# Kernel tuning notes

Measured on AMD Instinct MI355X. Metric: run time of the kernel, lower is better.

Reference implementation:

```python
import jax, jax.numpy as jnp
import numpy as np

B, T, D = 4, 1024, 1024
NEXP, TOPK = 8, 2
N = B * T
# eval capacity: floor(TOPK * 2.0 * N / NEXP) = 2048, already even and >= min_capacity
CAP = 2048
LN_EPS = 1e-5


def setup_inputs() -> dict:
    key = jax.random.key(0)
    ks = jax.random.split(key, 4)
    x = jax.random.normal(ks[0], (B, T, D), jnp.float32)
    w_g = jax.random.normal(ks[1], (D, NEXP), jnp.float32) * 0.02
    c_fc = jax.random.normal(ks[2], (NEXP, D, 4 * D), jnp.float32) * 0.02
    c_proj = jax.random.normal(ks[3], (NEXP, 4 * D, D), jnp.float32) * 0.02
    ln_w = jnp.ones((D,), jnp.float32)
    ln_b = jnp.zeros((D,), jnp.float32)
    return {"x": x, "w_g": w_g, "c_fc": c_fc, "c_proj": c_proj, "ln_w": ln_w, "ln_b": ln_b}


def moe_forward(x, w_g, c_fc, c_proj, ln_w, ln_b):
    xf = x.reshape(N, D)
    # --- Router ---
    logits = xf @ w_g                                   # [N, E]
    topk_vals, topk_idx = jax.lax.top_k(logits, TOPK)   # [N, K]
    masked = jnp.full_like(logits, -jnp.inf)
    masked = masked.at[jnp.arange(N)[:, None], topk_idx].set(topk_vals)
    probs = jax.nn.softmax(masked, axis=-1)             # [N, E]

    # capacity-based ranking (slot 0 for all tokens first, then slot 1, ...)
    onehot = jax.nn.one_hot(topk_idx, NEXP, dtype=jnp.int32)     # [N, K, E]
    exp_mask = jnp.transpose(onehot, (1, 0, 2))                  # [K, N, E]
    rank = jnp.cumsum(exp_mask.reshape(TOPK * N, NEXP), axis=0) - 1
    rank = rank.reshape(TOPK, N, NEXP)
    exp_mask = exp_mask * (rank < CAP).astype(jnp.int32)         # drop overflow
    rank_tok = jnp.sum(exp_mask * rank, axis=-1)                 # [K, N]
    exp_w = exp_mask.astype(probs.dtype) * probs[None]           # [K, N, E]
    rank_oh = jax.nn.one_hot(rank_tok, CAP, dtype=probs.dtype)   # [K, N, C]
    cb_weight = jnp.einsum('kne,knc->nec', exp_w, rank_oh)       # [N, E, C]
    sec_mask = (cb_weight != 0).astype(x.dtype)                  # dispatch mask

    # --- dispatch -> experts -> combine ---
    xb = jnp.einsum('nec,nd->ecd', sec_mask, xf)                 # [E, C, D]
    h = jax.nn.gelu(jnp.einsum('ecd,edf->ecf', xb, c_fc), approximate=False)
    eo = jnp.einsum('ecf,efd->ecd', h, c_proj)                   # [E, C, D]
    out = jnp.einsum('nec,ecd->nd', cb_weight, eo)               # [N, D]

    # --- LayerNorm ---
    mu = out.mean(-1, keepdims=True)
    var = out.var(-1, keepdims=True)
    out = (out - mu) / jnp.sqrt(var + LN_EPS) * ln_w + ln_b
    return out.reshape(B, T, D)


def reference(x, w_g, c_fc, c_proj, ln_w, ln_b):
    return moe_forward(x, w_g, c_fc, c_proj, ln_w, ln_b)
```

## Files before the change

kernel.cpp:

```cpp
#include <hip/hip_runtime.h>
#include <math.h>

#define NEXP 8
#define CAP 2048
#define NTOK 4096
#define DDIM 1024
#define FDIM 4096

typedef __bf16 bf16x8 __attribute__((ext_vector_type(8)));
typedef float f32x4 __attribute__((ext_vector_type(4)));
typedef unsigned short u16x8 __attribute__((ext_vector_type(8)));

__device__ __forceinline__ unsigned short f2bf(float f) {
    unsigned int u = __float_as_uint(f);
    u += 0x7FFFu + ((u >> 16) & 1u);
    return (unsigned short)(u >> 16);
}
__device__ __forceinline__ float bf2f(unsigned short h) {
    return __uint_as_float(((unsigned int)h) << 16);
}

__device__ __forceinline__ void gld_lds16(const void* g, void* l) {
    __builtin_amdgcn_global_load_lds((const __attribute__((address_space(1))) void*)g,
                                     (__attribute__((address_space(3))) void*)l, 16, 0, 0);
}

__global__ __launch_bounds__(256) void transpose_cvt64(const float* __restrict__ in,
                                                       unsigned short* __restrict__ out,
                                                       int R, int C) {
    __shared__ float tile[64][65];
    int e = blockIdx.z;
    const float* ip = in + (size_t)e * R * C;
    unsigned short* op = out + (size_t)e * R * C;
    int c0 = blockIdx.x * 64, r0 = blockIdx.y * 64;
    int t = threadIdx.x;
#pragma unroll
    for (int i = 0; i < 4; i++) {
        int rr = i * 16 + (t >> 4);
        int cc = (t & 15) * 4;
        float4 v = *(const float4*)&ip[(size_t)(r0 + rr) * C + c0 + cc];
        tile[rr][cc] = v.x; tile[rr][cc + 1] = v.y; tile[rr][cc + 2] = v.z; tile[rr][cc + 3] = v.w;
    }
    __syncthreads();
    int c = t >> 2, rb = (t & 3) * 16;
    u16x8 o0, o1;
#pragma unroll
    for (int j = 0; j < 8; j++) o0[j] = f2bf(tile[rb + j][c]);
#pragma unroll
    for (int j = 0; j < 8; j++) o1[j] = f2bf(tile[rb + 8 + j][c]);
    unsigned short* dst = op + (size_t)(c0 + c) * R + r0 + rb;
    *(u16x8*)dst = o0;
    *(u16x8*)(dst + 8) = o1;
}

__global__ __launch_bounds__(256) void router_kernel(const float* __restrict__ x,
                                                     const float* __restrict__ wg,
                                                     int2* __restrict__ e01,
                                                     float2* __restrict__ p01) {
    int wid = threadIdx.x >> 6, lane = threadIdx.x & 63;
    int n = blockIdx.x * 4 + wid;
    float acc[8];
#pragma unroll
    for (int i = 0; i < 8; i++) acc[i] = 0.f;
    const float4* xr = (const float4*)(x + (size_t)n * DDIM);
#pragma unroll
    for (int j = 0; j < 4; j++) {
        float4 xv = xr[j * 64 + lane];
        int base = (j * 64 + lane) * 4;
        float xs[4] = {xv.x, xv.y, xv.z, xv.w};
#pragma unroll
        for (int t = 0; t < 4; t++) {
            const float4* wr = (const float4*)(wg + (size_t)(base + t) * 8);
            float4 w0 = wr[0], w1 = wr[1];
            acc[0] += xs[t] * w0.x; acc[1] += xs[t] * w0.y;
            acc[2] += xs[t] * w0.z; acc[3] += xs[t] * w0.w;
            acc[4] += xs[t] * w1.x; acc[5] += xs[t] * w1.y;
            acc[6] += xs[t] * w1.z; acc[7] += xs[t] * w1.w;
        }
    }
#pragma unroll
    for (int off = 32; off > 0; off >>= 1) {
#pragma unroll
        for (int i = 0; i < 8; i++) acc[i] += __shfl_xor(acc[i], off);
    }
    if (lane == 0) {
        int i0 = 0; float v0 = acc[0];
#pragma unroll
        for (int q = 1; q < 8; q++) { if (acc[q] > v0) { v0 = acc[q]; i0 = q; } }
        int i1 = -1; float v1 = -3.0e38f;
#pragma unroll
        for (int q = 0; q < 8; q++) { if (q != i0 && acc[q] > v1) { v1 = acc[q]; i1 = q; } }
        float ea = expf(v0 - v0), eb = expf(v1 - v0);
        float inv = 1.f / (ea + eb);
        e01[n] = make_int2(i0, i1);
        p01[n] = make_float2(ea * inv, eb * inv);
    }
}

__global__ void assign_kernel(const int2* __restrict__ e01, int* __restrict__ counts,
                              int* __restrict__ assign_row, int* __restrict__ tok_slot) {
    int lane = threadIdx.x;
    int base[8];
#pragma unroll
    for (int i = 0; i < 8; i++) base[i] = 0;
    unsigned long long below = ((unsigned long long)1 << lane) - 1ull;
    int2 cur = e01[lane];
    for (int pass = 0; pass < 2; ++pass) {
        for (int t = 0; t < NTOK; t += 64) {
            int n = t + lane;
            int2 nxt;
            if (t + 64 < NTOK) nxt = e01[t + 64 + lane];
            else nxt = (pass == 0) ? e01[lane] : make_int2(0, 0);
            int ex = (pass == 0) ? cur.x : cur.y;
            int slot = -1;
#pragma unroll
            for (int q = 0; q < 8; q++) {
                unsigned long long m = __ballot(ex == q);
                if (ex == q) slot = base[q] + __popcll(m & below);
                base[q] += __popcll(m);
            }
            if (slot < CAP) {
                assign_row[ex * CAP + slot] = n;
                tok_slot[2 * n + pass] = slot;
            } else {
                tok_slot[2 * n + pass] = -1;
            }
            cur = nxt;
        }
    }
    if (lane < 8) counts[lane] = base[lane] > CAP ? CAP : base[lane];
}

__global__ __launch_bounds__(256) void gather_rows(const float* __restrict__ x,
                                                   const int* __restrict__ assign_row,
                                                   const int* __restrict__ counts,
                                                   unsigned short* __restrict__ xg) {
    int e = blockIdx.y;
    int wid = threadIdx.x >> 6, lane = threadIdx.x & 63;
    int slot = blockIdx.x * 4 + wid;
    if (slot >= counts[e]) return;
    int n = assign_row[e * CAP + slot];
    const float4* src = (const float4*)(x + (size_t)n * DDIM);
    unsigned short* dst = xg + ((size_t)e * CAP + slot) * DDIM;
#pragma unroll
    for (int j = 0; j < 4; j++) {
        float4 v = src[j * 64 + lane];
        ushort4 o;
        o.x = f2bf(v.x); o.y = f2bf(v.y); o.z = f2bf(v.z); o.w = f2bf(v.w);
        *(ushort4*)(dst + (size_t)(j * 64 + lane) * 4) = o;
    }
}

template <bool GELU, int KC>
__global__ __launch_bounds__(256, 4) void gemm_db(const unsigned short* __restrict__ A,
                                                  const unsigned short* __restrict__ Bt,
                                                  unsigned short* __restrict__ Cout,
                                                  const int* __restrict__ counts,
                                                  int Ncols, int Ktot) {
    constexpr int ABYTES = 8192;
    constexpr int BUFB = 16384;
    __shared__ __align__(16) char smem[2 * BUFB];

    int gx = gridDim.x, gy = gridDim.y;
    int nwg = gx * gy * gridDim.z;
    int flat = blockIdx.x + gx * (blockIdx.y + gy * blockIdx.z);
    int cpx = nwg >> 3;
    int swz = (flat & 7) * cpx + (flat >> 3);
    int gxy = gx * gy;
    int zz = swz / gxy;
    int r2 = swz - zz * gxy;
    int by = r2 / gx;
    int bx = r2 - by * gx;
    int e = zz / KC, kc = zz % KC;

    int cnt = counts[e];
    int row0 = by * 128;
    if (row0 >= cnt) return;
    int col0 = bx * 128;
    const int Ksub = Ktot / KC;
    const int NT = Ksub >> 5;

    int tid = threadIdx.x;
    int w = tid >> 6, lane = tid & 63;
    int wm = w >> 1, wn = w & 1;

    const unsigned short* Ab = A + ((size_t)e * CAP + row0) * Ktot + (size_t)kc * Ksub;
    const unsigned short* Bb = Bt + ((size_t)e * Ncols + col0) * Ktot + (size_t)kc * Ksub;

    int kel = (((tid & 3) ^ ((tid >> 3) & 3)) * 8);
    int rA = tid >> 2;
    int ldst = tid * 16;

    int a_off[4], b_off[4];
    int c = lane >> 4;
#pragma unroll
    for (int m = 0; m < 4; m++) {
        int row = wm * 64 + m * 16 + (lane & 15);
        a_off[m] = row * 64 + ((c ^ ((row >> 1) & 3)) * 16);
    }
#pragma unroll
    for (int n = 0; n < 4; n++) {
        int row = wn * 64 + n * 16 + (lane & 15);
        b_off[n] = row * 64 + ((c ^ ((row >> 1) & 3)) * 16);
    }

    auto stage = [&](int tt) {
        int bb = (tt & 1) * BUFB;
        size_t kt = (size_t)tt * 32 + kel;
#pragma unroll
        for (int i = 0; i < 2; i++)
            gld_lds16(Ab + (size_t)(i * 64 + rA) * Ktot + kt, smem + bb + i * 4096 + ldst);
#pragma unroll
        for (int i = 0; i < 2; i++)
            gld_lds16(Bb + (size_t)(i * 64 + rA) * Ktot + kt, smem + bb + ABYTES + i * 4096 + ldst);
    };

    f32x4 acc[4][4] = {};

    stage(0);
    __builtin_amdgcn_sched_barrier(0);
    __syncthreads();

    for (int t = 0; t < NT; ++t) {
        const int bb = (t & 1) * BUFB;
        if (t + 1 < NT) stage(t + 1);
        __builtin_amdgcn_sched_barrier(0);
        bf16x8 af[4], bfr[4];
#pragma unroll
        for (int m = 0; m < 4; m++) af[m] = *(const bf16x8*)(smem + bb + a_off[m]);
#pragma unroll
        for (int n = 0; n < 4; n++) bfr[n] = *(const bf16x8*)(smem + bb + ABYTES + b_off[n]);
        __builtin_amdgcn_s_setprio(1);
#pragma unroll
        for (int m = 0; m < 4; m++)
#pragma unroll
            for (int n = 0; n < 4; n++)
                acc[m][n] = __builtin_amdgcn_mfma_f32_16x16x32_bf16(af[m], bfr[n], acc[m][n], 0, 0, 0);
        __builtin_amdgcn_s_setprio(0);
        __syncthreads();
    }

    unsigned short* Cb = Cout + (((size_t)(kc * NEXP + e) * CAP + row0)) * Ncols + col0;
#pragma unroll
    for (int m = 0; m < 4; m++)
#pragma unroll
        for (int n = 0; n < 4; n++)
#pragma unroll
            for (int j = 0; j < 4; j++) {
                int lr = wm * 64 + m * 16 + ((lane >> 4) << 2) + j;
                int lc = wn * 64 + n * 16 + (lane & 15);
                float v = acc[m][n][j];
                if constexpr (GELU) {
                    float g = 0.5f * v * (1.0f + erff(v * 0.70710678118654752f));
                    Cb[(size_t)lr * Ncols + lc] = f2bf(g);
                } else {
                    Cb[(size_t)lr * Ncols + lc] = f2bf(v);
                }
            }
}

__global__ __launch_bounds__(256) void combine_ln_kernel(const unsigned short* __restrict__ pb,
                                                         const int2* __restrict__ e01,
                                                         const float2* __restrict__ p01,
                                                         const int* __restrict__ tok_slot,
                                                         const float* __restrict__ lnw,
                                                         const float* __restrict__ lnb,
                                                         float* __restrict__ out) {
    const size_t PLANE = (size_t)NEXP * CAP * DDIM;
    int n = blockIdx.x, t = threadIdx.x;
    int2 e = e01[n];
    float2 p = p01[n];
    int s0 = tok_slot[2 * n], s1 = tok_slot[2 * n + 1];
    float o0 = 0.f, o1 = 0.f, o2 = 0.f, o3 = 0.f;
    if (s0 >= 0) {
        size_t base = ((size_t)e.x * CAP + s0) * DDIM;
        ushort4 u0 = ((const ushort4*)(pb + base))[t];
        ushort4 u1 = ((const ushort4*)(pb + PLANE + base))[t];
        o0 += p.x * (bf2f(u0.x) + bf2f(u1.x));
        o1 += p.x * (bf2f(u0.y) + bf2f(u1.y));
        o2 += p.x * (bf2f(u0.z) + bf2f(u1.z));
        o3 += p.x * (bf2f(u0.w) + bf2f(u1.w));
    }
    if (s1 >= 0) {
        size_t base = ((size_t)e.y * CAP + s1) * DDIM;
        ushort4 u0 = ((const ushort4*)(pb + base))[t];
        ushort4 u1 = ((const ushort4*)(pb + PLANE + base))[t];
        o0 += p.y * (bf2f(u0.x) + bf2f(u1.x));
        o1 += p.y * (bf2f(u0.y) + bf2f(u1.y));
        o2 += p.y * (bf2f(u0.z) + bf2f(u1.z));
        o3 += p.y * (bf2f(u0.w) + bf2f(u1.w));
    }
    float s = o0 + o1 + o2 + o3;
    float sq = o0 * o0 + o1 * o1 + o2 * o2 + o3 * o3;
#pragma unroll
    for (int off = 32; off > 0; off >>= 1) {
        s += __shfl_xor(s, off);
        sq += __shfl_xor(sq, off);
    }
    __shared__ float red[8];
    int wid = t >> 6, lane = t & 63;
    if (lane == 0) { red[wid] = s; red[4 + wid] = sq; }
    __syncthreads();
    s = red[0] + red[1] + red[2] + red[3];
    sq = red[4] + red[5] + red[6] + red[7];
    float mu = s * (1.f / DDIM);
    float var = sq * (1.f / DDIM) - mu * mu;
    float inv = rsqrtf(var + 1e-5f);
    const float4 w = ((const float4*)lnw)[t];
    const float4 b = ((const float4*)lnb)[t];
    float4 r;
    r.x = (o0 - mu) * inv * w.x + b.x;
    r.y = (o1 - mu) * inv * w.y + b.y;
    r.z = (o2 - mu) * inv * w.z + b.z;
    r.w = (o3 - mu) * inv * w.w + b.w;
    ((float4*)(out + (size_t)n * DDIM))[t] = r;
}

extern "C" void kernel_launch(void* const* d_in, const int* in_sizes, int n_in,
                              void* d_out, int out_size, void* d_ws, size_t ws_size,
                              hipStream_t stream) {
    const float* x   = (const float*)d_in[0];
    const float* wg  = (const float*)d_in[1];
    const float* cfc = (const float*)d_in[2];
    const float* cpr = (const float*)d_in[3];
    const float* lnw = (const float*)d_in[4];
    const float* lnb = (const float*)d_in[5];
    float* out = (float*)d_out;

    char* ws = (char*)d_ws;
    size_t off = 0;
    auto take = [&](size_t b) {
        char* p = ws + off;
        off += (b + 255) & ~(size_t)255;
        return p;
    };
    unsigned short* cfct = (unsigned short*)take((size_t)NEXP * FDIM * DDIM * 2);
    unsigned short* pb = cfct;
    unsigned short* cprt = (unsigned short*)take((size_t)NEXP * DDIM * FDIM * 2);
    unsigned short* xg   = (unsigned short*)take((size_t)NEXP * CAP * DDIM * 2);
    unsigned short* h    = (unsigned short*)take((size_t)NEXP * CAP * FDIM * 2);
    int2*   e01      = (int2*)take(NTOK * sizeof(int2));
    float2* p01      = (float2*)take(NTOK * sizeof(float2));
    int*    tok_slot = (int*)take((size_t)NTOK * 2 * 4);
    int*    assign_row = (int*)take((size_t)NEXP * CAP * 4);
    int*    counts   = (int*)take(256);

    transpose_cvt64<<<dim3(FDIM / 64, DDIM / 64, NEXP), 256, 0, stream>>>(cfc, cfct, DDIM, FDIM);
    transpose_cvt64<<<dim3(DDIM / 64, FDIM / 64, NEXP), 256, 0, stream>>>(cpr, cprt, FDIM, DDIM);
    router_kernel<<<NTOK / 4, 256, 0, stream>>>(x, wg, e01, p01);
    assign_kernel<<<1, 64, 0, stream>>>(e01, counts, assign_row, tok_slot);
    gather_rows<<<dim3(CAP / 4, NEXP), 256, 0, stream>>>(x, assign_row, counts, xg);
    gemm_db<true, 1><<<dim3(FDIM / 128, CAP / 128, NEXP), 256, 0, stream>>>(xg, cfct, h, counts, FDIM, DDIM);
    gemm_db<false, 2><<<dim3(DDIM / 128, CAP / 128, NEXP * 2), 256, 0, stream>>>(h, cprt, pb, counts, DDIM, FDIM);
    combine_ln_kernel<<<NTOK, 256, 0, stream>>>(pb, e01, p01, tok_slot, lnw, lnb, out);
}
```

Baseline: 359.3 us.

## Use 256x256 tiles with 512 threads and triple-buffered LDS pipeline in expert GEMMs

The expert GEMM kernel now uses 256x256 output tiles with 8 waves per block, each wave holding an 8x4 grid of MFMA accumulators. LDS goes from two to three buffers, loads are issued two k-steps ahead, and explicit vmcnt waits with raw s_barrier replace __syncthreads. The intent is more data reuse per LDS load and better hiding of global-load latency. In exchange the block needs 96KB of LDS and uses more registers, so occupancy drops. The FDIM=4096 GEMM launches fewer blocks, which can hurt load balance on a GPU with many CUs.

```diff
diff --git a/kernel.cpp b/kernel.cpp
--- a/kernel.cpp
+++ b/kernel.cpp
@@ -152,14 +152,14 @@
 }
 
 template <bool GELU, int KC>
-__global__ __launch_bounds__(256, 4) void gemm_db(const unsigned short* __restrict__ A,
+__global__ __launch_bounds__(512, 2) void gemm_pc(const unsigned short* __restrict__ A,
                                                   const unsigned short* __restrict__ Bt,
                                                   unsigned short* __restrict__ Cout,
                                                   const int* __restrict__ counts,
                                                   int Ncols, int Ktot) {
-    constexpr int ABYTES = 8192;
-    constexpr int BUFB = 16384;
-    __shared__ __align__(16) char smem[2 * BUFB];
+    constexpr int ABYTES = 16384;
+    constexpr int BUFB = 32768;
+    __shared__ __align__(16) char smem[3 * BUFB];
 
     int gx = gridDim.x, gy = gridDim.y;
     int nwg = gx * gy * gridDim.z;
@@ -174,82 +174,82 @@
     int e = zz / KC, kc = zz % KC;
 
     int cnt = counts[e];
-    int row0 = by * 128;
+    int row0 = by * 256;
     if (row0 >= cnt) return;
-    int col0 = bx * 128;
+    int col0 = bx * 256;
     const int Ksub = Ktot / KC;
-    const int NT = Ksub >> 5;
-
-    int tid = threadIdx.x;
-    int w = tid >> 6, lane = tid & 63;
-    int wm = w >> 1, wn = w & 1;
+    const int NT = Ksub / 32;
+
+    int tid = threadIdx.x, w = tid >> 6, lane = tid & 63;
+    int wm = w >> 2, wn = w & 3;
 
     const unsigned short* Ab = A + ((size_t)e * CAP + row0) * Ktot + (size_t)kc * Ksub;
     const unsigned short* Bb = Bt + ((size_t)e * Ncols + col0) * Ktot + (size_t)kc * Ksub;
 
     int kel = (((tid & 3) ^ ((tid >> 3) & 3)) * 8);
-    int rA = tid >> 2;
-    int ldst = tid * 16;
-
-    int a_off[4], b_off[4];
-    int c = lane >> 4;
-#pragma unroll
-    for (int m = 0; m < 4; m++) {
-        int row = wm * 64 + m * 16 + (lane & 15);
-        a_off[m] = row * 64 + ((c ^ ((row >> 1) & 3)) * 16);
-    }
-#pragma unroll
-    for (int n = 0; n < 4; n++) {
-        int row = wn * 64 + n * 16 + (lane & 15);
-        b_off[n] = row * 64 + ((c ^ ((row >> 1) & 3)) * 16);
+    int aoff[8], boff[4];
+    int c0 = lane >> 4;
+#pragma unroll
+    for (int mq = 0; mq < 8; mq++) {
+        int row = wm * 128 + mq * 16 + (lane & 15);
+        aoff[mq] = row * 64 + ((c0 ^ ((row >> 1) & 3)) << 4);
+    }
+#pragma unroll
+    for (int nq = 0; nq < 4; nq++) {
+        int row = wn * 64 + nq * 16 + (lane & 15);
+        boff[nq] = row * 64 + ((c0 ^ ((row >> 1) & 3)) << 4);
     }
 
     auto stage = [&](int tt) {
-        int bb = (tt & 1) * BUFB;
+        int bb = (tt % 3) * BUFB;
         size_t kt = (size_t)tt * 32 + kel;
 #pragma unroll
         for (int i = 0; i < 2; i++)
-            gld_lds16(Ab + (size_t)(i * 64 + rA) * Ktot + kt, smem + bb + i * 4096 + ldst);
+            gld_lds16(Ab + (size_t)(i * 128 + (tid >> 2)) * Ktot + kt, smem + bb + i * 8192 + tid * 16);
 #pragma unroll
         for (int i = 0; i < 2; i++)
-            gld_lds16(Bb + (size_t)(i * 64 + rA) * Ktot + kt, smem + bb + ABYTES + i * 4096 + ldst);
+            gld_lds16(Bb + (size_t)(i * 128 + (tid >> 2)) * Ktot + kt, smem + bb + ABYTES + i * 8192 + tid * 16);
     };
 
-    f32x4 acc[4][4] = {};
-
-    stage(0);
+    f32x4 acc[8][4] = {};
+
+    stage(0); stage(1);
+    asm volatile("s_waitcnt vmcnt(4) lgkmcnt(0)" ::: "memory");
     __builtin_amdgcn_sched_barrier(0);
-    __syncthreads();
+    __builtin_amdgcn_s_barrier();
 
     for (int t = 0; t < NT; ++t) {
-        const int bb = (t & 1) * BUFB;
-        if (t + 1 < NT) stage(t + 1);
+        const int bb = (t % 3) * BUFB;
+        if (t + 2 < NT) stage(t + 2);
         __builtin_amdgcn_sched_barrier(0);
-        bf16x8 af[4], bfr[4];
-#pragma unroll
-        for (int m = 0; m < 4; m++) af[m] = *(const bf16x8*)(smem + bb + a_off[m]);
-#pragma unroll
-        for (int n = 0; n < 4; n++) bfr[n] = *(const bf16x8*)(smem + bb + ABYTES + b_off[n]);
+        bf16x8 a[8], b[4];
+#pragma unroll
+        for (int mq = 0; mq < 8; mq++) a[mq] = *(const bf16x8*)(smem + bb + aoff[mq]);
+#pragma unroll
+        for (int nq = 0; nq < 4; nq++) b[nq] = *(const bf16x8*)(smem + bb + ABYTES + boff[nq]);
         __builtin_amdgcn_s_setprio(1);
 #pragma unroll
-        for (int m = 0; m < 4; m++)
-#pragma unroll
-            for (int n = 0; n < 4; n++)
-                acc[m][n] = __builtin_amdgcn_mfma_f32_16x16x32_bf16(af[m], bfr[n], acc[m][n], 0, 0, 0);
+        for (int mq = 0; mq < 8; mq++)
+#pragma unroll
+            for (int nq = 0; nq < 4; nq++)
+                acc[mq][nq] = __builtin_amdgcn_mfma_f32_16x16x32_bf16(a[mq], b[nq], acc[mq][nq], 0, 0, 0);
         __builtin_amdgcn_s_setprio(0);
-        __syncthreads();
+        if (t + 2 < NT) asm volatile("s_waitcnt vmcnt(4) lgkmcnt(0)" ::: "memory");
+        else            asm volatile("s_waitcnt vmcnt(0) lgkmcnt(0)" ::: "memory");
+        __builtin_amdgcn_sched_barrier(0);
+        __builtin_amdgcn_s_barrier();
     }
 
     unsigned short* Cb = Cout + (((size_t)(kc * NEXP + e) * CAP + row0)) * Ncols + col0;
 #pragma unroll
-    for (int m = 0; m < 4; m++)
-#pragma unroll
-        for (int n = 0; n < 4; n++)
+    for (int mq = 0; mq < 8; mq++)
+#pragma unroll
+        for (int nq = 0; nq < 4; nq++)
 #pragma unroll
             for (int j = 0; j < 4; j++) {
-                int lr = wm * 64 + m * 16 + ((lane >> 4) << 2) + j;
-                int lc = wn * 64 + n * 16 + (lane & 15);
-                float v = acc[m][n][j];
+                int lr = wm * 128 + mq * 16 + ((lane >> 4) << 2) + j;
+                int lc = wn * 64 + nq * 16 + (lane & 15);
+                float v = acc[mq][nq][j];
                 if constexpr (GELU) {
                     float g = 0.5f * v * (1.0f + erff(v * 0.70710678118654752f));
                     Cb[(size_t)lr * Ncols + lc] = f2bf(g);
@@ -350,7 +350,7 @@
     router_kernel<<<NTOK / 4, 256, 0, stream>>>(x, wg, e01, p01);
     assign_kernel<<<1, 64, 0, stream>>>(e01, counts, assign_row, tok_slot);
     gather_rows<<<dim3(CAP / 4, NEXP), 256, 0, stream>>>(x, assign_row, counts, xg);
-    gemm_db<true, 1><<<dim3(FDIM / 128, CAP / 128, NEXP), 256, 0, stream>>>(xg, cfct, h, counts, FDIM, DDIM);
-    gemm_db<false, 2><<<dim3(DDIM / 128, CAP / 128, NEXP * 2), 256, 0, stream>>>(h, cprt, pb, counts, DDIM, FDIM);
+    gemm_pc<true, 1><<<dim3(FDIM / 256, CAP / 256, NEXP), 512, 0, stream>>>(xg, cfct, h, counts, FDIM, DDIM);
+    gemm_pc<false, 2><<<dim3(DDIM / 256, CAP / 256, NEXP * 2), 512, 0, stream>>>(h, cprt, pb, counts, DDIM, FDIM);
     combine_ln_kernel<<<NTOK, 256, 0, stream>>>(pb, e01, p01, tok_slot, lnw, lnb, out);
 }
```

Result: slower. 408.7 us (+13.7%).
